# Optimization experiments

Hardware: AMD Instinct MI355X
Metric: run time of the kernel (lower is better)

## Reference

```python
import jax, jax.numpy as jnp
import numpy as np

SEQ, BATCH, EMB, HID = 1024, 128, 512, 512

def setup_inputs() -> dict:
    key = jax.random.key(0)
    k1, k2 = jax.random.split(key)
    x = jax.random.normal(k1, (SEQ, BATCH, EMB), dtype=jnp.float32)
    # Linear(emb+hid -> 4*hid); store as [in, out] so we do z = cat(x,h) @ W + b
    W = jax.random.normal(k2, (EMB + HID, 4 * HID), dtype=jnp.float32) * (1.0 / np.sqrt(EMB + HID))
    b = jnp.zeros((4 * HID,), dtype=jnp.float32)
    return {"x": x, "W": W, "b": b}

def reference(x, W, b):
    # x: [seq, batch, emb]; one-layer unidirectional LSTM, gates in order i,f,g,o.
    B = x.shape[1]
    h0 = jnp.zeros((B, HID), dtype=x.dtype)
    c0 = jnp.zeros((B, HID), dtype=x.dtype)

    def step(carry, xt):
        h, c = carry
        z = jnp.concatenate([xt, h], axis=-1) @ W + b  # [batch, 4*hid]
        i, f, g, o = jnp.split(z, 4, axis=-1)
        c = jax.nn.sigmoid(f) * c + jax.nn.sigmoid(i) * jnp.tanh(g)
        h = jax.nn.sigmoid(o) * jnp.tanh(c)
        return (h, c), h

    (hT, cT), out = jax.lax.scan(step, (h0, c0), x)  # out: [seq, batch, hid]
    return out, (hT, cT)
```

## Files before the change

### kernel.cpp

```cpp
#include <hip/hip_runtime.h>
#include <hip/hip_bf16.h>

#define SEQ  1024
#define BATCH 128
#define EMB   512
#define HID   512
#define KDIM 1024
#define NZ   2048

typedef __bf16 bf16;
typedef __attribute__((ext_vector_type(8))) __bf16 bf16x8;
typedef __attribute__((ext_vector_type(4))) __bf16 bf16x4;
typedef __attribute__((ext_vector_type(4))) float f32x4;
typedef __attribute__((ext_vector_type(4))) unsigned int uint4v;

__global__ void convert_w(const float* __restrict__ W, bf16* __restrict__ Ws) {
    int idx = blockIdx.x * 256 + threadIdx.x;
    int k = idx >> 11;
    int n = idx & 2047;
    float w = W[idx];
    int kb = k >> 5, ko = k & 31;
    Ws[((kb * NZ + n) << 5) + ko] = (bf16)w;
}

__global__ __launch_bounds__(256) void lstm_step(
    const float* __restrict__ x,
    const bf16*  __restrict__ Ws,
    const float* __restrict__ bias,
    const bf16*  __restrict__ h_in,
    bf16*        __restrict__ h_out,
    float*       __restrict__ c,
    float*       __restrict__ out,
    int t)
{
    __shared__ bf16 Ash[16 * 1032];
    __shared__ float zsh[4][16][17];

    const int tid  = threadIdx.x;
    const int wave = tid >> 6;
    const int lane = tid & 63;
    const int ln   = lane & 15;
    const int q    = lane >> 4;

    const int gb = blockIdx.x >> 5;
    const int gc = blockIdx.x & 31;
    const int m0 = gb * 16;
    const int c0 = gc * 16;
    const int n0 = wave * 512 + c0;

    #pragma unroll
    for (int i = 0; i < 8; ++i) {
        int f4  = (tid + i * 256) * 4;
        int row = f4 >> 9;
        int kk  = f4 & 511;
        float4 v = *(const float4*)(x + ((size_t)t * BATCH + m0 + row) * EMB + kk);
        bf16x4 pv = { (bf16)v.x, (bf16)v.y, (bf16)v.z, (bf16)v.w };
        *(bf16x4*)&Ash[row * 1032 + kk] = pv;
    }
    if (t == 0) {
        #pragma unroll
        for (int i = 0; i < 4; ++i) {
            int e8  = (tid + i * 256) * 8;
            int row = e8 >> 9;
            int kk  = e8 & 511;
            uint4v z = {0u, 0u, 0u, 0u};
            *(uint4v*)&Ash[row * 1032 + 512 + kk] = z;
        }
    } else {
        #pragma unroll
        for (int i = 0; i < 4; ++i) {
            int e8  = (tid + i * 256) * 8;
            int row = e8 >> 9;
            int kk  = e8 & 511;
            *(uint4v*)&Ash[row * 1032 + 512 + kk] =
                *(const uint4v*)(h_in + (size_t)(m0 + row) * HID + kk);
        }
    }
    __syncthreads();

    f32x4 acc = {0.f, 0.f, 0.f, 0.f};
    #pragma unroll 8
    for (int kb = 0; kb < 32; ++kb) {
        bf16x8 a = *(const bf16x8*)&Ash[ln * 1032 + kb * 32 + q * 8];
        bf16x8 b = *(const bf16x8*)&Ws[((kb * NZ + n0 + ln) << 5) + q * 8];
        acc = __builtin_amdgcn_mfma_f32_16x16x32_bf16(a, b, acc, 0, 0, 0);
    }

    float bn = bias[n0 + ln];
    #pragma unroll
    for (int r = 0; r < 4; ++r)
        zsh[wave][q * 4 + r][ln] = acc[r] + bn;
    __syncthreads();

    int bl = tid >> 4;
    int hl = tid & 15;
    float zi = zsh[0][bl][hl];
    float zf = zsh[1][bl][hl];
    float zg = zsh[2][bl][hl];
    float zo = zsh[3][bl][hl];

    int gbatch = m0 + bl;
    int ghid   = c0 + hl;
    size_t cidx = (size_t)gbatch * HID + ghid;

    float c_old = (t == 0) ? 0.f : c[cidx];
    float si = 1.f / (1.f + __expf(-zi));
    float sf = 1.f / (1.f + __expf(-zf));
    float so = 1.f / (1.f + __expf(-zo));
    float tg = tanhf(zg);
    float cn = sf * c_old + si * tg;
    float hn = so * tanhf(cn);

    c[cidx]     = cn;
    h_out[cidx] = (bf16)hn;
    out[((size_t)t * BATCH + gbatch) * HID + ghid] = hn;
    if (t == SEQ - 1) {
        out[(size_t)SEQ * BATCH * HID + cidx] = hn;
        out[(size_t)SEQ * BATCH * HID + (size_t)BATCH * HID + cidx] = cn;
    }
}

extern "C" void kernel_launch(void* const* d_in, const int* in_sizes, int n_in,
                              void* d_out, int out_size, void* d_ws, size_t ws_size,
                              hipStream_t stream) {
    const float* x    = (const float*)d_in[0];
    const float* W    = (const float*)d_in[1];
    const float* bias = (const float*)d_in[2];
    float* out = (float*)d_out;

    char* ws = (char*)d_ws;
    bf16*  Ws = (bf16*)ws;
    bf16*  h0 = (bf16*)(ws + 4 * 1024 * 1024);
    bf16*  h1 = (bf16*)(ws + 4 * 1024 * 1024 + 128 * 1024);
    float* c  = (float*)(ws + 4 * 1024 * 1024 + 256 * 1024);

    convert_w<<<dim3(8192), dim3(256), 0, stream>>>(W, Ws);

    for (int t = 0; t < SEQ; ++t) {
        bf16* hin  = (t & 1) ? h1 : h0;
        bf16* hout = (t & 1) ? h0 : h1;
        lstm_step<<<dim3(256), dim3(256), 0, stream>>>(x, Ws, bias, hin, hout, c, out, t);
    }
}
```

Before: 6.390 ms.

## Replace per-timestep launches with persistent cooperative kernel and LDS-resident weights

Replaces 1024 per-step kernel launches with one cooperative persistent kernel that loops over time. Each block keeps its slice of the bf16 weight matrix in LDS and the cell state in registers, and blocks sharing a batch group synchronise through an atomic counter barrier in global memory. The tiling changes to 32 batch rows by 8 hidden columns per block, with a block-to-XCD mapping so each batch group's blocks share an XCD. This removes launch overhead and the per-step reload of weights from global memory, but adds spin-wait barrier latency and depends on all blocks being co-resident.

```diff
diff --git a/kernel.cpp b/kernel.cpp
--- a/kernel.cpp
+++ b/kernel.cpp
@@ -1,12 +1,11 @@
 #include <hip/hip_runtime.h>
-#include <hip/hip_bf16.h>
 
-#define SEQ  1024
+#define SEQ   1024
 #define BATCH 128
 #define EMB   512
 #define HID   512
-#define KDIM 1024
-#define NZ   2048
+#define KDIM  1024
+#define NZ    2048
 
 typedef __bf16 bf16;
 typedef __attribute__((ext_vector_type(8))) __bf16 bf16x8;
@@ -23,100 +22,130 @@
     Ws[((kb * NZ + n) << 5) + ko] = (bf16)w;
 }
 
-__global__ __launch_bounds__(256) void lstm_step(
+__global__ __launch_bounds__(256) void lstm_persist(
     const float* __restrict__ x,
     const bf16*  __restrict__ Ws,
     const float* __restrict__ bias,
-    const bf16*  __restrict__ h_in,
-    bf16*        __restrict__ h_out,
-    float*       __restrict__ c,
-    float*       __restrict__ out,
-    int t)
+    bf16* h0buf, bf16* h1buf,
+    unsigned int* bar,
+    float* __restrict__ out)
 {
-    __shared__ bf16 Ash[16 * 1032];
-    __shared__ float zsh[4][16][17];
+    __shared__ bf16  Wlds[2 * 32 * 64 * 8];
+    __shared__ bf16  Ash[32 * 1032];
+    __shared__ float zsh[32][33];
 
     const int tid  = threadIdx.x;
-    const int wave = tid >> 6;
     const int lane = tid & 63;
     const int ln   = lane & 15;
     const int q    = lane >> 4;
+    const int wave = tid >> 6;
+    const int mh   = wave & 1;
+    const int chh  = wave >> 1;
 
-    const int gb = blockIdx.x >> 5;
-    const int gc = blockIdx.x & 31;
-    const int m0 = gb * 16;
-    const int c0 = gc * 16;
-    const int n0 = wave * 512 + c0;
+    const int xcd = blockIdx.x & 7;
+    const int gb  = xcd >> 1;
+    const int gc  = (xcd & 1) * 32 + (blockIdx.x >> 3);
+    const int m0  = gb * 32;
+    const int hc0 = gc * 8;
 
     #pragma unroll
-    for (int i = 0; i < 8; ++i) {
-        int f4  = (tid + i * 256) * 4;
-        int row = f4 >> 9;
-        int kk  = f4 & 511;
-        float4 v = *(const float4*)(x + ((size_t)t * BATCH + m0 + row) * EMB + kk);
-        bf16x4 pv = { (bf16)v.x, (bf16)v.y, (bf16)v.z, (bf16)v.w };
-        *(bf16x4*)&Ash[row * 1032 + kk] = pv;
-    }
-    if (t == 0) {
-        #pragma unroll
-        for (int i = 0; i < 4; ++i) {
-            int e8  = (tid + i * 256) * 8;
-            int row = e8 >> 9;
-            int kk  = e8 & 511;
-            uint4v z = {0u, 0u, 0u, 0u};
-            *(uint4v*)&Ash[row * 1032 + 512 + kk] = z;
-        }
-    } else {
-        #pragma unroll
-        for (int i = 0; i < 4; ++i) {
-            int e8  = (tid + i * 256) * 8;
-            int row = e8 >> 9;
-            int kk  = e8 & 511;
-            *(uint4v*)&Ash[row * 1032 + 512 + kk] =
-                *(const uint4v*)(h_in + (size_t)(m0 + row) * HID + kk);
-        }
-    }
-    __syncthreads();
-
-    f32x4 acc = {0.f, 0.f, 0.f, 0.f};
-    #pragma unroll 8
-    for (int kb = 0; kb < 32; ++kb) {
-        bf16x8 a = *(const bf16x8*)&Ash[ln * 1032 + kb * 32 + q * 8];
-        bf16x8 b = *(const bf16x8*)&Ws[((kb * NZ + n0 + ln) << 5) + q * 8];
-        acc = __builtin_amdgcn_mfma_f32_16x16x32_bf16(a, b, acc, 0, 0, 0);
+    for (int i = 0; i < 16; ++i) {
+        int cI  = tid + i * 256;
+        int L2  = cI & 63;
+        int kb  = (cI >> 6) & 31;
+        int ch2 = cI >> 11;
+        int cc  = ch2 * 16 + (L2 & 15);
+        int n   = ((cc >> 3) << 9) + hc0 + (cc & 7);
+        *(uint4v*)&Wlds[cI * 8] =
+            *(const uint4v*)&Ws[((kb * NZ + n) << 5) + ((L2 >> 4) << 3)];
     }
 
-    float bn = bias[n0 + ln];
-    #pragma unroll
-    for (int r = 0; r < 4; ++r)
-        zsh[wave][q * 4 + r][ln] = acc[r] + bn;
-    __syncthreads();
+    const int ml = tid >> 3, hl = tid & 7;
+    const float bI = bias[        hc0 + hl];
+    const float bF = bias[ 512 + hc0 + hl];
+    const float bG = bias[1024 + hc0 + hl];
+    const float bO = bias[1536 + hc0 + hl];
+    const int gbatch = m0 + ml, ghid = hc0 + hl;
+    const size_t hidx = (size_t)gbatch * HID + ghid;
+    float c_reg = 0.f;
 
-    int bl = tid >> 4;
-    int hl = tid & 15;
-    float zi = zsh[0][bl][hl];
-    float zf = zsh[1][bl][hl];
-    float zg = zsh[2][bl][hl];
-    float zo = zsh[3][bl][hl];
+    unsigned int* cnt = bar + (gb << 5);
 
-    int gbatch = m0 + bl;
-    int ghid   = c0 + hl;
-    size_t cidx = (size_t)gbatch * HID + ghid;
+    for (int t = 0; t < SEQ; ++t) {
+        const bf16* h_in  = (t & 1) ? h1buf : h0buf;
+        bf16*       h_out = (t & 1) ? h0buf : h1buf;
 
-    float c_old = (t == 0) ? 0.f : c[cidx];
-    float si = 1.f / (1.f + __expf(-zi));
-    float sf = 1.f / (1.f + __expf(-zf));
-    float so = 1.f / (1.f + __expf(-zo));
-    float tg = tanhf(zg);
-    float cn = sf * c_old + si * tg;
-    float hn = so * tanhf(cn);
+        #pragma unroll
+        for (int i = 0; i < 16; ++i) {
+            int f4  = (tid + i * 256) * 4;
+            int row = f4 >> 9;
+            int kk  = f4 & 511;
+            float4 v = *(const float4*)(x + ((size_t)t * BATCH + m0 + row) * EMB + kk);
+            bf16x4 pv = { (bf16)v.x, (bf16)v.y, (bf16)v.z, (bf16)v.w };
+            *(bf16x4*)&Ash[row * 1032 + kk] = pv;
+        }
+        if (t == 0) {
+            #pragma unroll
+            for (int i = 0; i < 8; ++i) {
+                int e8  = (tid + i * 256) * 8;
+                int row = e8 >> 9;
+                int kk  = e8 & 511;
+                uint4v z = {0u, 0u, 0u, 0u};
+                *(uint4v*)&Ash[row * 1032 + 512 + kk] = z;
+            }
+        } else {
+            #pragma unroll
+            for (int i = 0; i < 8; ++i) {
+                int e8  = (tid + i * 256) * 8;
+                int row = e8 >> 9;
+                int kk  = e8 & 511;
+                *(uint4v*)&Ash[row * 1032 + 512 + kk] =
+                    *(const uint4v*)(h_in + (m0 + row) * HID + kk);
+            }
+        }
+        __syncthreads();
 
-    c[cidx]     = cn;
-    h_out[cidx] = (bf16)hn;
-    out[((size_t)t * BATCH + gbatch) * HID + ghid] = hn;
-    if (t == SEQ - 1) {
-        out[(size_t)SEQ * BATCH * HID + cidx] = hn;
-        out[(size_t)SEQ * BATCH * HID + (size_t)BATCH * HID + cidx] = cn;
+        f32x4 acc = {0.f, 0.f, 0.f, 0.f};
+        #pragma unroll 8
+        for (int kb = 0; kb < 32; ++kb) {
+            bf16x8 a = *(const bf16x8*)&Ash[(mh * 16 + ln) * 1032 + kb * 32 + q * 8];
+            bf16x8 b = *(const bf16x8*)&Wlds[(((chh * 32 + kb) << 6) + lane) << 3];
+            acc = __builtin_amdgcn_mfma_f32_16x16x32_bf16(a, b, acc, 0, 0, 0);
+        }
+        #pragma unroll
+        for (int r = 0; r < 4; ++r)
+            zsh[mh * 16 + q * 4 + r][chh * 16 + ln] = acc[r];
+        __syncthreads();
+
+        float zi = zsh[ml][     hl] + bI;
+        float zf = zsh[ml][ 8 + hl] + bF;
+        float zg = zsh[ml][16 + hl] + bG;
+        float zo = zsh[ml][24 + hl] + bO;
+        float si = 1.f / (1.f + __expf(-zi));
+        float sf = 1.f / (1.f + __expf(-zf));
+        float so = 1.f / (1.f + __expf(-zo));
+        float tg = tanhf(zg);
+        c_reg = sf * c_reg + si * tg;
+        float hn = so * tanhf(c_reg);
+
+        h_out[hidx] = (bf16)hn;
+        out[((size_t)t * BATCH + gbatch) * HID + ghid] = hn;
+        if (t == SEQ - 1) {
+            out[(size_t)SEQ * BATCH * HID + hidx] = hn;
+            out[(size_t)SEQ * BATCH * HID + (size_t)BATCH * HID + hidx] = c_reg;
+            break;
+        }
+
+        __syncthreads();
+        if (tid == 0) {
+            __threadfence();
+            __hip_atomic_fetch_add(cnt, 1u, __ATOMIC_RELEASE, __HIP_MEMORY_SCOPE_AGENT);
+            unsigned target = (unsigned)(t + 1) << 6;
+            while (__hip_atomic_load(cnt, __ATOMIC_RELAXED, __HIP_MEMORY_SCOPE_AGENT) < target)
+                ;
+            __threadfence();
+        }
+        __syncthreads();
     }
 }
 
@@ -129,16 +158,16 @@
     float* out = (float*)d_out;
 
     char* ws = (char*)d_ws;
-    bf16*  Ws = (bf16*)ws;
-    bf16*  h0 = (bf16*)(ws + 4 * 1024 * 1024);
-    bf16*  h1 = (bf16*)(ws + 4 * 1024 * 1024 + 128 * 1024);
-    float* c  = (float*)(ws + 4 * 1024 * 1024 + 256 * 1024);
+    bf16* Ws = (bf16*)ws;
+    bf16* h0 = (bf16*)(ws + (4 << 20));
+    bf16* h1 = (bf16*)(ws + (4 << 20) + (128 << 10));
+    unsigned int* cnt = (unsigned int*)(ws + (4 << 20) + (256 << 10));
 
+    hipMemsetAsync(cnt, 0, 4 * 128, stream);
     convert_w<<<dim3(8192), dim3(256), 0, stream>>>(W, Ws);
 
-    for (int t = 0; t < SEQ; ++t) {
-        bf16* hin  = (t & 1) ? h1 : h0;
-        bf16* hout = (t & 1) ? h0 : h1;
-        lstm_step<<<dim3(256), dim3(256), 0, stream>>>(x, Ws, bias, hin, hout, c, out, t);
-    }
+    void* args[] = { (void*)&x, (void*)&Ws, (void*)&bias,
+                     (void*)&h0, (void*)&h1, (void*)&cnt, (void*)&out };
+    hipLaunchCooperativeKernel((const void*)lstm_persist, dim3(256), dim3(256),
+                               args, 0, stream);
 }
```

Result: slower. 19.75 ms (+209.1%).
